# Performance work log

Measured on AMD Instinct MI355X. Metric: run time of the kernel, lower is better.

The kernel has to match this reference:

```python
import jax, jax.numpy as jnp
import numpy as np
from functools import partial

B, T, F = 4096, 256, 32
H1, H2, NT = 64, 32, 3


def _lstm_layer(x, W_ih, W_hh, b_ih, b_hh):
    """Torch-style LSTM (batch_first). x: [B,T,Fin], W_ih: [4H,Fin], W_hh: [4H,H].
    Gate order i, f, g, o. Returns all hidden states [B,T,H]."""
    Bsz = x.shape[0]
    H = W_hh.shape[1]
    # Precompute input contribution for all timesteps (one big GEMM)
    xg = jnp.einsum('btf,gf->btg', x, W_ih) + b_ih + b_hh  # [B,T,4H]

    def step(carry, xg_t):
        h, c = carry
        gates = xg_t + h @ W_hh.T  # [B,4H]
        i, f, g, o = jnp.split(gates, 4, axis=-1)
        i = jax.nn.sigmoid(i)
        f = jax.nn.sigmoid(f)
        g = jnp.tanh(g)
        o = jax.nn.sigmoid(o)
        c = f * c + i * g
        h = o * jnp.tanh(c)
        return (h, c), h

    init = (jnp.zeros((Bsz, H), x.dtype), jnp.zeros((Bsz, H), x.dtype))
    _, hs = jax.lax.scan(step, init, jnp.swapaxes(xg, 0, 1))  # hs: [T,B,H]
    return jnp.swapaxes(hs, 0, 1)


def setup_inputs() -> dict:
    key = jax.random.key(0)
    ks = jax.random.split(key, 12)
    s1 = 1.0 / np.sqrt(H1)
    s2 = 1.0 / np.sqrt(H2)
    u = lambda k, shape, s: jax.random.uniform(k, shape, jnp.float32, -s, s)
    return {
        'x': jax.random.normal(ks[0], (B, T, F), jnp.float32),
        'W_ih1': u(ks[1], (4 * H1, F), s1),
        'W_hh1': u(ks[2], (4 * H1, H1), s1),
        'b_ih1': u(ks[3], (4 * H1,), s1),
        'b_hh1': u(ks[4], (4 * H1,), s1),
        'W_ih2': u(ks[5], (4 * H2, H1), s2),
        'W_hh2': u(ks[6], (4 * H2, H2), s2),
        'b_ih2': u(ks[7], (4 * H2,), s2),
        'b_hh2': u(ks[8], (4 * H2,), s2),
        'W_head': u(ks[9], (NT, H2), s2),
        'b_head': u(ks[10], (NT,), s2),
    }


def reference(x, W_ih1, W_hh1, b_ih1, b_hh1, W_ih2, W_hh2, b_ih2, b_hh2, W_head, b_head):
    h1 = _lstm_layer(x, W_ih1, W_hh1, b_ih1, b_hh1)   # [B,T,64]; dropout is identity in eval
    h2 = _lstm_layer(h1, W_ih2, W_hh2, b_ih2, b_hh2)  # [B,T,32]
    last = h2[:, -1, :]                               # [B,32]
    return last @ W_head.T + b_head                   # [B,3]
```

## Files before the change

kernel.cpp:

```cpp
#include <hip/hip_runtime.h>

#define Bsz 4096
#define Tt  256
#define Ff  32
#define H1  64
#define H2  32
#define NTAPS 3
#define BT  16
#define NTHR 768

typedef _Float16 half8  __attribute__((ext_vector_type(8)));
typedef _Float16 half2v __attribute__((ext_vector_type(2)));
typedef float    f32x4  __attribute__((ext_vector_type(4)));

#define H1S 72
#define XS  40
#define H2S 40
#define HDS 33

__device__ __forceinline__ float fast_sigmoid(float x) {
    float e = __builtin_amdgcn_exp2f(-1.4426950408889634f * x);
    return __builtin_amdgcn_rcpf(1.0f + e);
}
__device__ __forceinline__ float fast_tanh(float x) {
    float ax = __builtin_fabsf(x);
    float e = __builtin_amdgcn_exp2f(-2.8853900817779268f * ax);
    float t = 1.0f - 2.0f * e * __builtin_amdgcn_rcpf(1.0f + e);
    return __builtin_copysignf(t, x);
}

#define MFMA16(a, b, c) __builtin_amdgcn_mfma_f32_16x16x32_f16((a), (b), (c), 0, 0, 0)

__global__ __launch_bounds__(NTHR, 3)
void lstm2_fused(const float* __restrict__ x,
                 const float* __restrict__ Wih1, const float* __restrict__ Whh1,
                 const float* __restrict__ bih1, const float* __restrict__ bhh1,
                 const float* __restrict__ Wih2, const float* __restrict__ Whh2,
                 const float* __restrict__ bih2, const float* __restrict__ bhh2,
                 const float* __restrict__ Whead, const float* __restrict__ bhead,
                 float* __restrict__ out)
{
    __shared__ __align__(16) _Float16 sH1[2][BT][H1S];
    __shared__ __align__(16) _Float16 sX [2][BT][XS];
    __shared__ __align__(16) _Float16 sH2[2][BT][H2S];
    __shared__ __align__(16) float    sHead[BT][HDS];

    const int tid  = threadIdx.x;
    const int wid  = tid >> 6;
    const int lane = tid & 63;
    const int l15  = lane & 15;
    const int q    = lane >> 4;
    const int b0   = blockIdx.x * BT;

    const bool isL1 = (wid < 8);
    const int  hg   = isL1 ? (wid >> 1) : ((wid - 8) >> 1);
    const int  hf   = wid & 1;
    const int  r0   = 2 * hf, r1 = r0 + 1;

    half8 w[4][3];
    float bias[4];
    if (isL1) {
        #pragma unroll
        for (int G = 0; G < 4; ++G) {
            int gr = G * 64 + hg * 16 + l15;
            #pragma unroll
            for (int c = 0; c < 3; ++c) {
                half8 v;
                #pragma unroll
                for (int e = 0; e < 8; ++e) {
                    int k = c * 32 + q * 8 + e;
                    float f = (k < H1) ? Whh1[gr * H1 + k] : Wih1[gr * Ff + (k - H1)];
                    v[e] = (_Float16)f;
                }
                w[G][c] = v;
            }
            bias[G] = bih1[gr] + bhh1[gr];
        }
    } else {
        #pragma unroll
        for (int G = 0; G < 4; ++G) {
            int gr = G * 32 + hg * 16 + l15;
            #pragma unroll
            for (int c = 0; c < 3; ++c) {
                half8 v;
                #pragma unroll
                for (int e = 0; e < 8; ++e) {
                    int kk = q * 8 + e;
                    float f = (c == 0) ? Whh2[gr * H2 + kk]
                                       : Wih2[gr * H1 + (c - 1) * 32 + kk];
                    v[e] = (_Float16)f;
                }
                w[G][c] = v;
            }
            bias[G] = bih2[gr] + bhh2[gr];
        }
    }

    for (int idx = tid; idx < BT * H1S; idx += NTHR) ((_Float16*)sH1[1])[idx] = (_Float16)0.0f;
    for (int idx = tid; idx < BT * H2S; idx += NTHR) ((_Float16*)sH2[1])[idx] = (_Float16)0.0f;

    float2 rA, rB;
    int xb = 0, xf = 0;
    if (tid >= 512) {
        int t = tid - 512;
        xb = t >> 4; xf = (t & 15) * 2;
        const float* xp = x + ((size_t)(b0 + xb) * Tt) * Ff + xf;
        float2 v0 = *(const float2*)xp;
        half2v h0; h0[0] = (_Float16)v0.x; h0[1] = (_Float16)v0.y;
        *(half2v*)&sX[0][xb][xf] = h0;
        rA = *(const float2*)(xp + 1 * Ff);
        rB = *(const float2*)(xp + 2 * Ff);
    }
    __syncthreads();

    float cs0 = 0.0f, cs1 = 0.0f;

    for (int i = 0; i <= Tt; ++i) {
        const int cur = i & 1, nxt = cur ^ 1;
        const bool active = isL1 ? (i < Tt) : (i >= 1);

        if (active) {
            half8 a0 = *(const half8*)&sH1[nxt][l15][q * 8];
            half8 a1 = *(const half8*)&sH1[nxt][l15][32 + q * 8];
            half8 A0, A1, A2;
            if (isL1) {
                half8 ax = *(const half8*)&sX[cur][l15][q * 8];
                A0 = a0; A1 = a1; A2 = ax;
            } else {
                half8 ah = *(const half8*)&sH2[cur][l15][q * 8];
                A0 = ah; A1 = a0; A2 = a1;
            }
            f32x4 acc[4];
            #pragma unroll
            for (int G = 0; G < 4; ++G) {
                f32x4 a = {bias[G], bias[G], bias[G], bias[G]};
                a = MFMA16(A0, w[G][0], a);
                a = MFMA16(A1, w[G][1], a);
                a = MFMA16(A2, w[G][2], a);
                acc[G] = a;
            }

            _Float16* hdst; int rs;
            if (isL1) { hdst = &sH1[cur][0][hg * 16 + l15]; rs = H1S; }
            else      { hdst = &sH2[nxt][0][hg * 16 + l15]; rs = H2S; }

            {
                float i_ = fast_sigmoid(acc[0][r0]);
                float f_ = fast_sigmoid(acc[1][r0]);
                float g_ = fast_tanh   (acc[2][r0]);
                float o_ = fast_sigmoid(acc[3][r0]);
                cs0 = f_ * cs0 + i_ * g_;
                float hh = o_ * fast_tanh(cs0);
                hdst[(q * 4 + r0) * rs] = (_Float16)hh;
                if (!isL1 && i == Tt) sHead[q * 4 + r0][hg * 16 + l15] = hh;
            }
            {
                float i_ = fast_sigmoid(acc[0][r1]);
                float f_ = fast_sigmoid(acc[1][r1]);
                float g_ = fast_tanh   (acc[2][r1]);
                float o_ = fast_sigmoid(acc[3][r1]);
                cs1 = f_ * cs1 + i_ * g_;
                float hh = o_ * fast_tanh(cs1);
                hdst[(q * 4 + r1) * rs] = (_Float16)hh;
                if (!isL1 && i == Tt) sHead[q * 4 + r1][hg * 16 + l15] = hh;
            }
        }

        if (tid >= 512) {
            if (i + 1 < Tt) {
                half2v hx; hx[0] = (_Float16)rA.x; hx[1] = (_Float16)rA.y;
                *(half2v*)&sX[nxt][xb][xf] = hx;
            }
            rA = rB;
            int tld = (i + 3 < Tt) ? (i + 3) : (Tt - 1);
            rB = *(const float2*)(x + ((size_t)(b0 + xb) * Tt + tld) * Ff + xf);
        }
        __syncthreads();
    }

    if (tid < BT * NTAPS) {
        int b = tid / NTAPS, n = tid - b * NTAPS;
        float s = bhead[n];
        #pragma unroll
        for (int k = 0; k < H2; ++k) s = fmaf(sHead[b][k], Whead[n * H2 + k], s);
        out[(size_t)(b0 + b) * NTAPS + n] = s;
    }
}

extern "C" void kernel_launch(void* const* d_in, const int* in_sizes, int n_in,
                              void* d_out, int out_size, void* d_ws, size_t ws_size,
                              hipStream_t stream) {
    const float* xp    = (const float*)d_in[0];
    const float* Wih1  = (const float*)d_in[1];
    const float* Whh1  = (const float*)d_in[2];
    const float* bih1  = (const float*)d_in[3];
    const float* bhh1  = (const float*)d_in[4];
    const float* Wih2  = (const float*)d_in[5];
    const float* Whh2  = (const float*)d_in[6];
    const float* bih2  = (const float*)d_in[7];
    const float* bhh2  = (const float*)d_in[8];
    const float* Whead = (const float*)d_in[9];
    const float* bhead = (const float*)d_in[10];
    float* outp = (float*)d_out;

    hipLaunchKernelGGL(lstm2_fused, dim3(Bsz / BT), dim3(NTHR), 0, stream,
                       xp, Wih1, Whh1, bih1, bhh1, Wih2, Whh2, bih2, bhh2,
                       Whead, bhead, outp);
}
```

Before: 430.7 us.

## Halve batch tile to 8 rows and fuse LSTM gate activations

Shrinks each block from 16 to 8 batch rows and 12 to 6 waves, so each wave now covers a full 16-column hidden slice. The 16-row MFMA tile is padded by duplicating the 8 batch rows, and lanes are remapped so each lane updates two distinct batch rows. This doubles the number of blocks to give more parallelism and fewer waves per barrier, at the cost of wasting half of each MFMA on duplicate rows. The gate math is also merged into one routine that pairs sigmoid*tanh products under a shared reciprocal, which cuts the count of rcp instructions.

```diff
diff --git a/kernel.cpp b/kernel.cpp
--- a/kernel.cpp
+++ b/kernel.cpp
@@ -6,8 +6,8 @@
 #define H1  64
 #define H2  32
 #define NTAPS 3
-#define BT  16
-#define NTHR 768
+#define BT  8
+#define NTHR 384
 
 typedef _Float16 half8  __attribute__((ext_vector_type(8)));
 typedef _Float16 half2v __attribute__((ext_vector_type(2)));
@@ -18,15 +18,20 @@
 #define H2S 40
 #define HDS 33
 
-__device__ __forceinline__ float fast_sigmoid(float x) {
-    float e = __builtin_amdgcn_exp2f(-1.4426950408889634f * x);
-    return __builtin_amdgcn_rcpf(1.0f + e);
-}
-__device__ __forceinline__ float fast_tanh(float x) {
-    float ax = __builtin_fabsf(x);
-    float e = __builtin_amdgcn_exp2f(-2.8853900817779268f * ax);
-    float t = 1.0f - 2.0f * e * __builtin_amdgcn_rcpf(1.0f + e);
-    return __builtin_copysignf(t, x);
+__device__ __forceinline__ float lstm_unit(float pi, float pf, float pg, float po,
+                                           float& c) {
+    const float K1 = 1.4426950408889634f;
+    float ei = __builtin_amdgcn_exp2f(-K1 * pi);
+    float ef = __builtin_amdgcn_exp2f(-K1 * pf);
+    float eg = __builtin_amdgcn_exp2f(-2.0f * K1 * __builtin_fabsf(pg));
+    float eo = __builtin_amdgcn_exp2f(-K1 * po);
+    float f_ = __builtin_amdgcn_rcpf(1.0f + ef);
+    float ig = (1.0f - eg) * __builtin_amdgcn_rcpf((1.0f + ei) * (1.0f + eg));
+    ig = __builtin_copysignf(ig, pg);
+    c = f_ * c + ig;
+    float ec = __builtin_amdgcn_exp2f(-2.0f * K1 * __builtin_fabsf(c));
+    float th = (1.0f - ec) * __builtin_amdgcn_rcpf((1.0f + eo) * (1.0f + ec));
+    return __builtin_copysignf(th, c);
 }
 
 #define MFMA16(a, b, c) __builtin_amdgcn_mfma_f32_16x16x32_f16((a), (b), (c), 0, 0, 0)
@@ -50,12 +55,15 @@
     const int lane = tid & 63;
     const int l15  = lane & 15;
     const int q    = lane >> 4;
+    const int row8 = l15 & 7;
     const int b0   = blockIdx.x * BT;
 
-    const bool isL1 = (wid < 8);
-    const int  hg   = isL1 ? (wid >> 1) : ((wid - 8) >> 1);
-    const int  hf   = wid & 1;
-    const int  r0   = 2 * hf, r1 = r0 + 1;
+    const bool isL1 = (wid < 4);
+    const int  hg   = isL1 ? wid : (wid - 4);
+
+    const int r0  = (q >> 1) * 2, r1 = r0 + 1;
+    const int bLo = (q & 1) * 4 + (q >> 1) * 2;
+    const int col = hg * 16 + l15;
 
     half8 w[4][3];
     float bias[4];
@@ -101,8 +109,8 @@
 
     float2 rA, rB;
     int xb = 0, xf = 0;
-    if (tid >= 512) {
-        int t = tid - 512;
+    if (tid >= 256) {
+        int t = tid - 256;
         xb = t >> 4; xf = (t & 15) * 2;
         const float* xp = x + ((size_t)(b0 + xb) * Tt) * Ff + xf;
         float2 v0 = *(const float2*)xp;
@@ -120,14 +128,14 @@
         const bool active = isL1 ? (i < Tt) : (i >= 1);
 
         if (active) {
-            half8 a0 = *(const half8*)&sH1[nxt][l15][q * 8];
-            half8 a1 = *(const half8*)&sH1[nxt][l15][32 + q * 8];
+            half8 a0 = *(const half8*)&sH1[nxt][row8][q * 8];
+            half8 a1 = *(const half8*)&sH1[nxt][row8][32 + q * 8];
             half8 A0, A1, A2;
             if (isL1) {
-                half8 ax = *(const half8*)&sX[cur][l15][q * 8];
+                half8 ax = *(const half8*)&sX[cur][row8][q * 8];
                 A0 = a0; A1 = a1; A2 = ax;
             } else {
-                half8 ah = *(const half8*)&sH2[cur][l15][q * 8];
+                half8 ah = *(const half8*)&sH2[cur][row8][q * 8];
                 A0 = ah; A1 = a0; A2 = a1;
             }
             f32x4 acc[4];
@@ -140,33 +148,20 @@
                 acc[G] = a;
             }
 
-            _Float16* hdst; int rs;
-            if (isL1) { hdst = &sH1[cur][0][hg * 16 + l15]; rs = H1S; }
-            else      { hdst = &sH2[nxt][0][hg * 16 + l15]; rs = H2S; }
-
-            {
-                float i_ = fast_sigmoid(acc[0][r0]);
-                float f_ = fast_sigmoid(acc[1][r0]);
-                float g_ = fast_tanh   (acc[2][r0]);
-                float o_ = fast_sigmoid(acc[3][r0]);
-                cs0 = f_ * cs0 + i_ * g_;
-                float hh = o_ * fast_tanh(cs0);
-                hdst[(q * 4 + r0) * rs] = (_Float16)hh;
-                if (!isL1 && i == Tt) sHead[q * 4 + r0][hg * 16 + l15] = hh;
-            }
-            {
-                float i_ = fast_sigmoid(acc[0][r1]);
-                float f_ = fast_sigmoid(acc[1][r1]);
-                float g_ = fast_tanh   (acc[2][r1]);
-                float o_ = fast_sigmoid(acc[3][r1]);
-                cs1 = f_ * cs1 + i_ * g_;
-                float hh = o_ * fast_tanh(cs1);
-                hdst[(q * 4 + r1) * rs] = (_Float16)hh;
-                if (!isL1 && i == Tt) sHead[q * 4 + r1][hg * 16 + l15] = hh;
-            }
-        }
-
-        if (tid >= 512) {
+            float h0 = lstm_unit(acc[0][r0], acc[1][r0], acc[2][r0], acc[3][r0], cs0);
+            float h1v = lstm_unit(acc[0][r1], acc[1][r1], acc[2][r1], acc[3][r1], cs1);
+
+            if (isL1) {
+                sH1[cur][bLo][col]     = (_Float16)h0;
+                sH1[cur][bLo + 1][col] = (_Float16)h1v;
+            } else {
+                sH2[nxt][bLo][col]     = (_Float16)h0;
+                sH2[nxt][bLo + 1][col] = (_Float16)h1v;
+                if (i == Tt) { sHead[bLo][col] = h0; sHead[bLo + 1][col] = h1v; }
+            }
+        }
+
+        if (tid >= 256) {
             if (i + 1 < Tt) {
                 half2v hx; hx[0] = (_Float16)rA.x; hx[1] = (_Float16)rA.y;
                 *(half2v*)&sX[nxt][xb][xf] = hx;
```

After: 470.4 us. 1.09x slower.
